# Performance work log

Hardware: AMD Instinct MI355X
Metric: run time of the kernel (lower is better)

## Reference

```python
import jax, jax.numpy as jnp
import numpy as np

N = 50000      # nodes
E = 640000     # edges
HID = 64       # hid_dim (per-head channels C)
HEADS = 4
D = HID * HEADS  # 256, conv output dim (concat=True)
LN_EPS = 1e-5


def setup_inputs() -> dict:
    key = jax.random.key(0)
    ks = jax.random.split(key, 10)
    def w(k, shape, scale=0.05):
        return jax.random.normal(k, shape, dtype=jnp.float32) * scale
    x = jax.random.normal(ks[0], (N, HID), dtype=jnp.float32)
    edge_index = jax.random.randint(ks[1], (2, E), 0, N)
    return {
        'x': x,
        'edge_index': edge_index,
        'Wq': w(ks[2], (D, HID)), 'bq': jnp.zeros((D,), jnp.float32),
        'Wk': w(ks[3], (D, HID)), 'bk': jnp.zeros((D,), jnp.float32),
        'Wv': w(ks[4], (D, HID)), 'bv': jnp.zeros((D,), jnp.float32),
        'Wskip': w(ks[5], (D, HID)), 'bskip': jnp.zeros((D,), jnp.float32),
        'Wbeta': w(ks[6], (1, 3 * D)),
        'ln_g': jnp.ones((D,), jnp.float32), 'ln_b': jnp.zeros((D,), jnp.float32),
        'Wproj': w(ks[7], (HID, D)), 'bproj': jnp.zeros((HID,), jnp.float32),
    }


def _layer(x, edge_index, Wq, bq, Wk, bk, Wv, bv, Wskip, bskip, Wbeta, ln_g, ln_b, Wproj, bproj):
    src, dst = edge_index[0], edge_index[1]  # message flows src -> dst
    # q/k/v projections, [N, H, C]
    q = (x @ Wq.T + bq).reshape(N, HEADS, HID)
    k = (x @ Wk.T + bk).reshape(N, HEADS, HID)
    v = (x @ Wv.T + bv).reshape(N, HEADS, HID)
    # edge-wise attention logits: [E, H]
    alpha = jnp.einsum('ehc,ehc->eh', q[dst], k[src]) / jnp.sqrt(jnp.float32(HID))
    # per-destination-node softmax (segment softmax)
    m = jax.ops.segment_max(alpha, dst, num_segments=N)          # [N, H]
    ex = jnp.exp(alpha - m[dst])                                 # [E, H]
    s = jax.ops.segment_sum(ex, dst, num_segments=N)             # [N, H]
    attn = ex / (s[dst] + 1e-16)                                 # [E, H]
    # weighted scatter-aggregate of values -> [N, H*C]
    msg = (v[src] * attn[..., None]).reshape(E, D)
    out = jax.ops.segment_sum(msg, dst, num_segments=N)          # [N, D]
    # beta gated skip (TransformerConv beta=True, root_weight=True)
    x_r = x @ Wskip.T + bskip                                    # [N, D]
    beta = jax.nn.sigmoid(jnp.concatenate([out, x_r, out - x_r], axis=-1) @ Wbeta.T)  # [N, 1]
    h = beta * x_r + (1.0 - beta) * out
    # LayerNorm over last dim
    mu = jnp.mean(h, axis=-1, keepdims=True)
    var = jnp.var(h, axis=-1, keepdims=True)
    h = (h - mu) * jax.lax.rsqrt(var + LN_EPS) * ln_g + ln_b
    # projection + residual + ReLU (dropout = identity in eval)
    h = h @ Wproj.T + bproj
    return jax.nn.relu(h + x)


def reference(x, edge_index, Wq, bq, Wk, bk, Wv, bv, Wskip, bskip, Wbeta, ln_g, ln_b, Wproj, bproj):
    return _layer(x, edge_index, Wq, bq, Wk, bk, Wv, bv, Wskip, bskip, Wbeta, ln_g, ln_b, Wproj, bproj)
```

## Files before the change

### kernel.cpp

```cpp
#include <hip/hip_runtime.h>
#include <stdint.h>

#define NND 50000
#define NED 640000

typedef unsigned short u16;
typedef unsigned int u32;
typedef __attribute__((ext_vector_type(8))) short short8;
typedef __attribute__((ext_vector_type(4))) float f32x4;
typedef __attribute__((ext_vector_type(2))) float fx2;

__device__ __forceinline__ float bf2f(u16 u) {
    union { u32 i; float f; } x; x.i = ((u32)u) << 16; return x.f;
}
__device__ __forceinline__ u16 f2bf(float f) {
    union { u32 i; float f; } x; x.f = f;
    u32 u = x.i;
    return (u16)((u + 0x7fffu + ((u >> 16) & 1u)) >> 16);
}
__device__ __forceinline__ float bflo(u32 w) {
    union { u32 i; float f; } x; x.i = w << 16; return x.f;
}
__device__ __forceinline__ float bfhi(u32 w) {
    union { u32 i; float f; } x; x.i = w & 0xffff0000u; return x.f;
}
__device__ __forceinline__ u32 pk2(float lo, float hi) {
    return (u32)f2bf(lo) | ((u32)f2bf(hi) << 16);
}
__device__ __forceinline__ u32 pk_fp8_4(u32 w0, u32 w1) {
    u32 p = __builtin_amdgcn_cvt_pk_fp8_f32(bflo(w0), bfhi(w0), 0, false);
    p = __builtin_amdgcn_cvt_pk_fp8_f32(bflo(w1), bfhi(w1), p, true);
    return p;
}
__device__ __forceinline__ void dec8v(u32 a, u32 b, fx2* f) {
    f[0] = __builtin_amdgcn_cvt_pk_f32_fp8(a, false);
    f[1] = __builtin_amdgcn_cvt_pk_f32_fp8(a, true);
    f[2] = __builtin_amdgcn_cvt_pk_f32_fp8(b, false);
    f[3] = __builtin_amdgcn_cvt_pk_f32_fp8(b, true);
}

__global__ void k_wt(const float* __restrict__ Wq, const float* __restrict__ Wk,
                     const float* __restrict__ Wv, const float* __restrict__ Ws,
                     const float* __restrict__ Wp,
                     const float* __restrict__ bq, const float* __restrict__ bk,
                     const float* __restrict__ bv, const float* __restrict__ bs,
                     u16* __restrict__ wb, float* __restrict__ bias_c,
                     u16* __restrict__ wpA, int* __restrict__ deg) {
    int idx = blockIdx.x * 256 + threadIdx.x;
    if (idx < 65536) {
        int j = idx & 7;
        int lane = (idx >> 3) & 63;
        int q = (idx >> 9) & 1;
        int dt = idx >> 10;
        int dim = dt * 16 + (lane & 15);
        int k = q * 32 + ((lane >> 4) & 3) * 8 + j;
        int mat = dim >> 8, r = dim & 255;
        const float* W = (mat == 0) ? Wq : (mat == 1) ? Wk : (mat == 2) ? Wv : Ws;
        float v = W[r * 64 + k] * ((mat == 0) ? 0.125f : 1.0f);
        wb[idx] = f2bf(v);
    } else if (idx < 65536 + 1024) {
        int dim = idx - 65536;
        int mat = dim >> 8, r = dim & 255;
        const float* B = (mat == 0) ? bq : (mat == 1) ? bk : (mat == 2) ? bv : bs;
        bias_c[dim] = B[r] * ((mat == 0) ? 0.125f : 1.0f);
    } else if (idx < 65536 + 1024 + 16384) {
        int w = idx - 66560;
        int j = w & 7;
        int lane = (w >> 3) & 63;
        int kc = (w >> 9) & 7;
        int mt = w >> 12;
        int dim = mt * 16 + (lane & 15);
        int k = kc * 32 + ((lane >> 4) & 3) * 8 + j;
        wpA[w] = f2bf(Wp[dim * 256 + k]);
    } else if (idx < 65536 + 1024 + 16384 + NND) {
        deg[idx - 82944] = 0;
    }
}

#define CNT_BLKS 2500
#define PPAD 1040
__global__ __launch_bounds__(256) void k_fillproj(
    const int* __restrict__ esrc, const int* __restrict__ edst,
    int* __restrict__ deg, int* __restrict__ csr,
    const float* __restrict__ x, const u16* __restrict__ wb,
    const float* __restrict__ bias_c,
    uint2* __restrict__ q8, uint4* __restrict__ kv8, u16* __restrict__ xr16)
{
    __shared__ u16 hb[16 * PPAD];
    if (blockIdx.x < CNT_BLKS) {
        int e = blockIdx.x * 256 + threadIdx.x;
        if (e < NED) {
            int d = edst[e];
            int pos = atomicAdd(&deg[d], 1);
            if (pos < 64) csr[(d << 6) + pos] = esrc[e];
        }
        return;
    }
    const int t = threadIdx.x;
    const int wave = t >> 6, lane = t & 63;
    const int node0 = (blockIdx.x - CNT_BLKS) * 16;
    const int lr = lane & 15, quad = lane >> 4;

    int node = node0 + lr;
    if (node > NND - 1) node = NND - 1;
    short8 xf0, xf1;
    {
        const float* xp = x + (size_t)node * 64 + quad * 8;
        float4 a = *reinterpret_cast<const float4*>(xp);
        float4 b = *reinterpret_cast<const float4*>(xp + 4);
        float4 c = *reinterpret_cast<const float4*>(xp + 32);
        float4 d = *reinterpret_cast<const float4*>(xp + 36);
        xf0[0] = (short)f2bf(a.x); xf0[1] = (short)f2bf(a.y);
        xf0[2] = (short)f2bf(a.z); xf0[3] = (short)f2bf(a.w);
        xf0[4] = (short)f2bf(b.x); xf0[5] = (short)f2bf(b.y);
        xf0[6] = (short)f2bf(b.z); xf0[7] = (short)f2bf(b.w);
        xf1[0] = (short)f2bf(c.x); xf1[1] = (short)f2bf(c.y);
        xf1[2] = (short)f2bf(c.z); xf1[3] = (short)f2bf(c.w);
        xf1[4] = (short)f2bf(d.x); xf1[5] = (short)f2bf(d.y);
        xf1[6] = (short)f2bf(d.z); xf1[7] = (short)f2bf(d.w);
    }
    #pragma unroll 4
    for (int dtl = 0; dtl < 16; ++dtl) {
        int dt = wave * 16 + dtl;
        const u16* wp = wb + (size_t)(dt * 2) * 512 + lane * 8;
        short8 a0 = *reinterpret_cast<const short8*>(wp);
        short8 a1 = *reinterpret_cast<const short8*>(wp + 512);
        f32x4 bias = *reinterpret_cast<const f32x4*>(bias_c + dt * 16 + quad * 4);
        f32x4 acc = {0.f, 0.f, 0.f, 0.f};
        acc = __builtin_amdgcn_mfma_f32_16x16x32_bf16(a0, xf0, acc, 0, 0, 0);
        acc = __builtin_amdgcn_mfma_f32_16x16x32_bf16(a1, xf1, acc, 0, 0, 0);
        uint2 st;
        st.x = pk2(acc[0] + bias[0], acc[1] + bias[1]);
        st.y = pk2(acc[2] + bias[2], acc[3] + bias[3]);
        *reinterpret_cast<uint2*>(&hb[lr * PPAD + dt * 16 + quad * 4]) = st;
    }
    __syncthreads();
    #pragma unroll
    for (int it = 0; it < 2; ++it) {
        int idx = it * 256 + t;
        int nip = idx >> 5, g = idx & 31;
        int gnode = node0 + nip;
        if (gnode < NND) {
            const u16* hp = &hb[nip * PPAD];
            *reinterpret_cast<uint4*>(xr16 + (size_t)gnode * 256 + g * 8) =
                *reinterpret_cast<const uint4*>(hp + 768 + g * 8);
            uint4 qw = *reinterpret_cast<const uint4*>(hp + g * 8);
            uint2 qs;
            qs.x = pk_fp8_4(qw.x, qw.y);
            qs.y = pk_fp8_4(qw.z, qw.w);
            q8[(size_t)gnode * 32 + g] = qs;
            uint4 kw = *reinterpret_cast<const uint4*>(hp + 256 + g * 8);
            uint4 vw = *reinterpret_cast<const uint4*>(hp + 512 + g * 8);
            uint4 kvs;
            kvs.x = pk_fp8_4(kw.x, kw.y);
            kvs.y = pk_fp8_4(kw.z, kw.w);
            kvs.z = pk_fp8_4(vw.x, vw.y);
            kvs.w = pk_fp8_4(vw.z, vw.w);
            kv8[(size_t)gnode * 32 + g] = kvs;
        }
    }
}

#define PS 264
#define NPB 16
__global__ __launch_bounds__(256) void k_attnepi(
    const int* __restrict__ deg, const int* __restrict__ csr,
    const uint2* __restrict__ q8, const uint4* __restrict__ kv8,
    const u16* __restrict__ xr16, const float* __restrict__ x,
    const float* __restrict__ Wbeta, const float* __restrict__ ln_g,
    const float* __restrict__ ln_b, const u16* __restrict__ wpA,
    const float* __restrict__ bproj, float* __restrict__ y)
{
    __shared__ u16 hn[NPB * PS];
    const int t = threadIdx.x;
    const int wave = __builtin_amdgcn_readfirstlane(t >> 6);
    const int lane = t & 63;
    const int sub = lane & 31, h = lane >> 5;
    const int es = (sub >> 4) & 1, dl = sub & 15;
    const int lr = lane & 15, grp = lane >> 4;
    const int base = blockIdx.x * NPB;

    int dg_[2], ia_[2], ib_[2];
    uint4 qv_[2];
    #pragma unroll
    for (int p = 0; p < 2; ++p) {
        int node = base + wave * 4 + 2 * p + h;
        int dgv = deg[node];
        dg_[p] = dgv > 64 ? 64 : dgv;
        ia_[p] = csr[(node << 6) + sub];
        ib_[p] = csr[(node << 6) + 32 + sub];
        qv_[p] = *reinterpret_cast<const uint4*>(
            reinterpret_cast<const char*>(q8) + (size_t)node * 256 + dl * 16);
    }
    const uint4* kvb = kv8 + (dl << 1);
    #pragma unroll
    for (int p = 0; p < 2; ++p) {
        const int dg = dg_[p];
        const int ia = ia_[p], ib = ib_[p];
        fx2 q[8];
        dec8v(qv_[p].x, qv_[p].y, q);
        dec8v(qv_[p].z, qv_[p].w, q + 4);
        int dgo = __shfl_xor(dg, 32);
        int mdg = __builtin_amdgcn_readfirstlane(dg > dgo ? dg : dgo);

        float s = 0.f;
        fx2 acc[8];
        #pragma unroll
        for (int r = 0; r < 8; ++r) acc[r] = fx2{0.f, 0.f};

        auto fetch = [&](int i, uint4& c0, uint4& c1) {
            int j = i + es;
            int lsrc = (h << 5) | (j & 31);
            int r0 = __shfl(ia, lsrc);
            int r1 = __shfl(ib, lsrc);
            int e = (j & 32) ? r1 : r0;
            if ((u32)e >= NND) e = 0;
            const uint4* kp = kvb + ((size_t)e << 5);
            c0 = kp[0];
            c1 = kp[1];
        };
        auto process = [&](int i, uint4 c0, uint4 c1) {
            int j = i + es;
            fx2 kk[8];
            dec8v(c0.x, c0.y, kk);
            dec8v(c1.x, c1.y, kk + 4);
            fx2 d0 = q[0] * kk[0] + q[1] * kk[1];
            fx2 d1 = q[2] * kk[2] + q[3] * kk[3];
            fx2 d2 = q[4] * kk[4] + q[5] * kk[5];
            fx2 d3 = q[6] * kk[6] + q[7] * kk[7];
            fx2 dd = (d0 + d1) + (d2 + d3);
            float pa = dd.x + dd.y;
            pa += __shfl_xor(pa, 1);
            pa += __shfl_xor(pa, 2);
            float ea = __expf(pa);
            ea = (j < dg) ? ea : 0.f;
            s += ea;
            fx2 ev = {ea, ea};
            fx2 vv[8];
            dec8v(c0.z, c0.w, vv);
            dec8v(c1.z, c1.w, vv + 4);
            acc[0] += ev * vv[0]; acc[1] += ev * vv[1];
            acc[2] += ev * vv[2]; acc[3] += ev * vv[3];
            acc[4] += ev * vv[4]; acc[5] += ev * vv[5];
            acc[6] += ev * vv[6]; acc[7] += ev * vv[7];
        };

        if (mdg > 0) {
            uint4 c0, c1, n0, n1;
            fetch(0, c0, c1);
            int i = 0;
            for (; i + 2 < mdg; i += 2) {
                fetch(i + 2, n0, n1);
                process(i, c0, c1);
                c0 = n0; c1 = n1;
            }
            process(i, c0, c1);
        }
        #pragma unroll
        for (int r = 0; r < 8; ++r) {
            acc[r].x += __shfl_xor(acc[r].x, 16);
            acc[r].y += __shfl_xor(acc[r].y, 16);
        }
        s += __shfl_xor(s, 16);
        float inv = 1.0f / (s + 1e-16f);
        if (es == 0) {
            int lid = wave * 4 + 2 * p + h;
            uint4 s0, s1;
            s0.x = pk2(acc[0].x * inv, acc[0].y * inv);
            s0.y = pk2(acc[1].x * inv, acc[1].y * inv);
            s0.z = pk2(acc[2].x * inv, acc[2].y * inv);
            s0.w = pk2(acc[3].x * inv, acc[3].y * inv);
            s1.x = pk2(acc[4].x * inv, acc[4].y * inv);
            s1.y = pk2(acc[5].x * inv, acc[5].y * inv);
            s1.z = pk2(acc[6].x * inv, acc[6].y * inv);
            s1.w = pk2(acc[7].x * inv, acc[7].y * inv);
            *reinterpret_cast<uint4*>(&hn[lid * PS + dl * 16]) = s0;
            *reinterpret_cast<uint4*>(&hn[lid * PS + dl * 16 + 8]) = s1;
        }
    }
    __syncthreads();

    {
        const float4* wb4 = reinterpret_cast<const float4*>(Wbeta);
        const float4* g44 = reinterpret_cast<const float4*>(ln_g);
        const float4* b44 = reinterpret_cast<const float4*>(ln_b);
        float wo[16], wx[16], wd[16], gg[16], bb[16];
        #pragma unroll
        for (int j = 0; j < 4; ++j) {
            float4 a = wb4[lr * 4 + j];
            float4 b = wb4[64 + lr * 4 + j];
            float4 c = wb4[128 + lr * 4 + j];
            float4 g = g44[lr * 4 + j];
            float4 bl = b44[lr * 4 + j];
            wo[j*4+0]=a.x; wo[j*4+1]=a.y; wo[j*4+2]=a.z; wo[j*4+3]=a.w;
            wx[j*4+0]=b.x; wx[j*4+1]=b.y; wx[j*4+2]=b.z; wx[j*4+3]=b.w;
            wd[j*4+0]=c.x; wd[j*4+1]=c.y; wd[j*4+2]=c.z; wd[j*4+3]=c.w;
            gg[j*4+0]=g.x; gg[j*4+1]=g.y; gg[j*4+2]=g.z; gg[j*4+3]=g.w;
            bb[j*4+0]=bl.x; bb[j*4+1]=bl.y; bb[j*4+2]=bl.z; bb[j*4+3]=bl.w;
        }
        int lid = wave * 4 + grp;
        int node = base + lid;
        {
            uint4 u0 = *reinterpret_cast<const uint4*>(&hn[lid * PS + lr * 16]);
            uint4 u1 = *reinterpret_cast<const uint4*>(&hn[lid * PS + lr * 16 + 8]);
            const uint4* xp = reinterpret_cast<const uint4*>(xr16 + (size_t)node * 256 + lr * 16);
            uint4 v0 = xp[0], v1 = xp[1];
            float o[16], r[16];
            o[0]=bflo(u0.x); o[1]=bfhi(u0.x); o[2]=bflo(u0.y); o[3]=bfhi(u0.y);
            o[4]=bflo(u0.z); o[5]=bfhi(u0.z); o[6]=bflo(u0.w); o[7]=bfhi(u0.w);
            o[8]=bflo(u1.x); o[9]=bfhi(u1.x); o[10]=bflo(u1.y); o[11]=bfhi(u1.y);
            o[12]=bflo(u1.z); o[13]=bfhi(u1.z); o[14]=bflo(u1.w); o[15]=bfhi(u1.w);
            r[0]=bflo(v0.x); r[1]=bfhi(v0.x); r[2]=bflo(v0.y); r[3]=bfhi(v0.y);
            r[4]=bflo(v0.z); r[5]=bfhi(v0.z); r[6]=bflo(v0.w); r[7]=bfhi(v0.w);
            r[8]=bflo(v1.x); r[9]=bfhi(v1.x); r[10]=bflo(v1.y); r[11]=bfhi(v1.y);
            r[12]=bflo(v1.z); r[13]=bfhi(v1.z); r[14]=bflo(v1.w); r[15]=bfhi(v1.w);
            float part = 0.f;
            #pragma unroll
            for (int cc = 0; cc < 16; ++cc)
                part = fmaf(wo[cc], o[cc], fmaf(wx[cc], r[cc], fmaf(wd[cc], o[cc]-r[cc], part)));
            part += __shfl_xor(part, 1); part += __shfl_xor(part, 2);
            part += __shfl_xor(part, 4); part += __shfl_xor(part, 8);
            float beta = 1.0f / (1.0f + __expf(-part));
            float hh[16];
            float sh = 0.f, sq = 0.f;
            #pragma unroll
            for (int cc = 0; cc < 16; ++cc) {
                hh[cc] = beta * r[cc] + (1.f - beta) * o[cc];
                sh += hh[cc];
                sq = fmaf(hh[cc], hh[cc], sq);
            }
            sh += __shfl_xor(sh, 1); sh += __shfl_xor(sh, 2);
            sh += __shfl_xor(sh, 4); sh += __shfl_xor(sh, 8);
            sq += __shfl_xor(sq, 1); sq += __shfl_xor(sq, 2);
            sq += __shfl_xor(sq, 4); sq += __shfl_xor(sq, 8);
            float mu = sh * (1.0f / 256.0f);
            float var = sq * (1.0f / 256.0f) - mu * mu;
            float ri = rsqrtf(var + 1e-5f);
            u32 pw[8];
            #pragma unroll
            for (int pp = 0; pp < 8; ++pp) {
                float z0 = (hh[pp*2+0] - mu) * ri * gg[pp*2+0] + bb[pp*2+0];
                float z1 = (hh[pp*2+1] - mu) * ri * gg[pp*2+1] + bb[pp*2+1];
                pw[pp] = pk2(z0, z1);
            }
            uint4 s0, s1;
            s0.x = pw[0]; s0.y = pw[1]; s0.z = pw[2]; s0.w = pw[3];
            s1.x = pw[4]; s1.y = pw[5]; s1.z = pw[6]; s1.w = pw[7];
            *reinterpret_cast<uint4*>(&hn[lid * PS + lr * 16]) = s0;
            *reinterpret_cast<uint4*>(&hn[lid * PS + lr * 16 + 8]) = s1;
        }
    }
    __syncthreads();

    {
        const int mt = wave;
        f32x4 acc = {0.f, 0.f, 0.f, 0.f};
        #pragma unroll
        for (int kc = 0; kc < 8; ++kc) {
            short8 a = *reinterpret_cast<const short8*>(wpA + ((size_t)(mt * 8 + kc) * 64 + lane) * 8);
            short8 b = *reinterpret_cast<const short8*>(&hn[lr * PS + kc * 32 + grp * 8]);
            acc = __builtin_amdgcn_mfma_f32_16x16x32_bf16(a, b, acc, 0, 0, 0);
        }
        int node = base + lr;
        {
            int d0 = mt * 16 + grp * 4;
            float4 bp4 = *reinterpret_cast<const float4*>(bproj + d0);
            float4 xv = *reinterpret_cast<const float4*>(x + (size_t)node * 64 + d0);
            float4 rr;
            rr.x = fmaxf(acc[0] + bp4.x + xv.x, 0.f);
            rr.y = fmaxf(acc[1] + bp4.y + xv.y, 0.f);
            rr.z = fmaxf(acc[2] + bp4.z + xv.z, 0.f);
            rr.w = fmaxf(acc[3] + bp4.w + xv.w, 0.f);
            *reinterpret_cast<float4*>(y + (size_t)node * 64 + d0) = rr;
        }
    }
}

extern "C" void kernel_launch(void* const* d_in, const int* in_sizes, int n_in,
                              void* d_out, int out_size, void* d_ws, size_t ws_size,
                              hipStream_t stream) {
    const float* x     = (const float*)d_in[0];
    const int*   eidx  = (const int*)d_in[1];
    const float* Wq    = (const float*)d_in[2];
    const float* bq    = (const float*)d_in[3];
    const float* Wk    = (const float*)d_in[4];
    const float* bk    = (const float*)d_in[5];
    const float* Wv    = (const float*)d_in[6];
    const float* bv    = (const float*)d_in[7];
    const float* Wsk   = (const float*)d_in[8];
    const float* bsk   = (const float*)d_in[9];
    const float* Wbeta = (const float*)d_in[10];
    const float* lng   = (const float*)d_in[11];
    const float* lnb   = (const float*)d_in[12];
    const float* Wp    = (const float*)d_in[13];
    const float* bp    = (const float*)d_in[14];
    float* y = (float*)d_out;

    char* ws = (char*)d_ws;
    size_t off = 0;
    auto alloc = [&](size_t b) { size_t o = off; off += (b + 255) & ~(size_t)255; return o; };
    uint2* q8   = (uint2*)(ws + alloc((size_t)NND * 256));
    uint4* kv8  = (uint4*)(ws + alloc((size_t)NND * 512));
    u16*  xr16  = (u16*)(ws + alloc((size_t)NND * 512));
    int* deg    = (int*)(ws + alloc((size_t)NND * 4));
    int* csr    = (int*)(ws + alloc((size_t)NND * 64 * 4));
    u16* wb     = (u16*)(ws + alloc((size_t)65536 * 2));
    float* bias_c = (float*)(ws + alloc((size_t)1024 * 4));
    u16* wpA    = (u16*)(ws + alloc((size_t)16384 * 2));

    k_wt      <<<520, 256, 0, stream>>>(Wq, Wk, Wv, Wsk, Wp, bq, bk, bv, bsk,
                                        wb, bias_c, wpA, deg);
    k_fillproj<<<CNT_BLKS + (NND + 15) / 16, 256, 0, stream>>>(
                 eidx, eidx + NED, deg, csr, x, wb, bias_c, q8, kv8, xr16);
    k_attnepi <<<(NND + NPB - 1) / NPB, 256, 0, stream>>>(deg, csr, q8, kv8, xr16, x,
                                                          Wbeta, lng, lnb, wpA, bp, y);
}
```

Before: 225.9 us.

## Shrink CSR to 16-bit indices, split K/V buffers, halve projection LDS

Stores the CSR neighbour indices as 16-bit values (node ids below 65536), so each node's adjacency list is fetched with one int load per lane and less memory traffic. The interleaved K/V fp8 buffer is split into separate K and V arrays, and the gather now issues one 16-byte load from each instead of two from the combined row. The projection kernel does its work in two passes through a half-size LDS tile (Q/K first, then V/skip), adding a barrier but lowering shared-memory use so more blocks can be resident. Bounds clamps are removed, so tail nodes rely on N being a multiple of 16, and the 16-bit ids only work while N stays below 65536.

```diff
diff --git a/kernel.cpp b/kernel.cpp
--- a/kernel.cpp
+++ b/kernel.cpp
@@ -10,9 +10,6 @@
 typedef __attribute__((ext_vector_type(4))) float f32x4;
 typedef __attribute__((ext_vector_type(2))) float fx2;
 
-__device__ __forceinline__ float bf2f(u16 u) {
-    union { u32 i; float f; } x; x.i = ((u32)u) << 16; return x.f;
-}
 __device__ __forceinline__ u16 f2bf(float f) {
     union { u32 i; float f; } x; x.f = f;
     u32 u = x.i;
@@ -78,21 +75,22 @@
 }
 
 #define CNT_BLKS 2500
-#define PPAD 1040
+#define PH 520
 __global__ __launch_bounds__(256) void k_fillproj(
     const int* __restrict__ esrc, const int* __restrict__ edst,
-    int* __restrict__ deg, int* __restrict__ csr,
+    int* __restrict__ deg, u16* __restrict__ csr,
     const float* __restrict__ x, const u16* __restrict__ wb,
     const float* __restrict__ bias_c,
-    uint2* __restrict__ q8, uint4* __restrict__ kv8, u16* __restrict__ xr16)
+    uint2* __restrict__ q8, uint2* __restrict__ k8, uint2* __restrict__ v8,
+    u16* __restrict__ xr16)
 {
-    __shared__ u16 hb[16 * PPAD];
+    __shared__ u16 hb[16 * PH];
     if (blockIdx.x < CNT_BLKS) {
         int e = blockIdx.x * 256 + threadIdx.x;
         if (e < NED) {
             int d = edst[e];
             int pos = atomicAdd(&deg[d], 1);
-            if (pos < 64) csr[(d << 6) + pos] = esrc[e];
+            if (pos < 64) csr[(d << 6) + pos] = (u16)esrc[e];
         }
         return;
     }
@@ -102,7 +100,6 @@
     const int lr = lane & 15, quad = lane >> 4;
 
     int node = node0 + lr;
-    if (node > NND - 1) node = NND - 1;
     short8 xf0, xf1;
     {
         const float* xp = x + (size_t)node * 64 + quad * 8;
@@ -119,9 +116,10 @@
         xf1[4] = (short)f2bf(d.x); xf1[5] = (short)f2bf(d.y);
         xf1[6] = (short)f2bf(d.z); xf1[7] = (short)f2bf(d.w);
     }
+
     #pragma unroll 4
-    for (int dtl = 0; dtl < 16; ++dtl) {
-        int dt = wave * 16 + dtl;
+    for (int dtl = 0; dtl < 8; ++dtl) {
+        int dt = wave * 8 + dtl;
         const u16* wp = wb + (size_t)(dt * 2) * 512 + lane * 8;
         short8 a0 = *reinterpret_cast<const short8*>(wp);
         short8 a1 = *reinterpret_cast<const short8*>(wp + 512);
@@ -132,7 +130,7 @@
         uint2 st;
         st.x = pk2(acc[0] + bias[0], acc[1] + bias[1]);
         st.y = pk2(acc[2] + bias[2], acc[3] + bias[3]);
-        *reinterpret_cast<uint2*>(&hb[lr * PPAD + dt * 16 + quad * 4]) = st;
+        *reinterpret_cast<uint2*>(&hb[lr * PH + dt * 16 + quad * 4]) = st;
     }
     __syncthreads();
     #pragma unroll
@@ -140,32 +138,58 @@
         int idx = it * 256 + t;
         int nip = idx >> 5, g = idx & 31;
         int gnode = node0 + nip;
-        if (gnode < NND) {
-            const u16* hp = &hb[nip * PPAD];
-            *reinterpret_cast<uint4*>(xr16 + (size_t)gnode * 256 + g * 8) =
-                *reinterpret_cast<const uint4*>(hp + 768 + g * 8);
-            uint4 qw = *reinterpret_cast<const uint4*>(hp + g * 8);
-            uint2 qs;
-            qs.x = pk_fp8_4(qw.x, qw.y);
-            qs.y = pk_fp8_4(qw.z, qw.w);
-            q8[(size_t)gnode * 32 + g] = qs;
-            uint4 kw = *reinterpret_cast<const uint4*>(hp + 256 + g * 8);
-            uint4 vw = *reinterpret_cast<const uint4*>(hp + 512 + g * 8);
-            uint4 kvs;
-            kvs.x = pk_fp8_4(kw.x, kw.y);
-            kvs.y = pk_fp8_4(kw.z, kw.w);
-            kvs.z = pk_fp8_4(vw.x, vw.y);
-            kvs.w = pk_fp8_4(vw.z, vw.w);
-            kv8[(size_t)gnode * 32 + g] = kvs;
-        }
+        const u16* hp = &hb[nip * PH];
+        uint4 qw = *reinterpret_cast<const uint4*>(hp + g * 8);
+        uint2 qs;
+        qs.x = pk_fp8_4(qw.x, qw.y);
+        qs.y = pk_fp8_4(qw.z, qw.w);
+        q8[(size_t)gnode * 32 + g] = qs;
+        uint4 kw = *reinterpret_cast<const uint4*>(hp + 256 + g * 8);
+        uint2 ks;
+        ks.x = pk_fp8_4(kw.x, kw.y);
+        ks.y = pk_fp8_4(kw.z, kw.w);
+        k8[(size_t)gnode * 32 + g] = ks;
+    }
+    __syncthreads();
+
+    #pragma unroll 4
+    for (int dtl = 0; dtl < 8; ++dtl) {
+        int dtg = 32 + wave * 8 + dtl;
+        const u16* wp = wb + (size_t)(dtg * 2) * 512 + lane * 8;
+        short8 a0 = *reinterpret_cast<const short8*>(wp);
+        short8 a1 = *reinterpret_cast<const short8*>(wp + 512);
+        f32x4 bias = *reinterpret_cast<const f32x4*>(bias_c + dtg * 16 + quad * 4);
+        f32x4 acc = {0.f, 0.f, 0.f, 0.f};
+        acc = __builtin_amdgcn_mfma_f32_16x16x32_bf16(a0, xf0, acc, 0, 0, 0);
+        acc = __builtin_amdgcn_mfma_f32_16x16x32_bf16(a1, xf1, acc, 0, 0, 0);
+        uint2 st;
+        st.x = pk2(acc[0] + bias[0], acc[1] + bias[1]);
+        st.y = pk2(acc[2] + bias[2], acc[3] + bias[3]);
+        *reinterpret_cast<uint2*>(&hb[lr * PH + (dtg - 32) * 16 + quad * 4]) = st;
+    }
+    __syncthreads();
+    #pragma unroll
+    for (int it = 0; it < 2; ++it) {
+        int idx = it * 256 + t;
+        int nip = idx >> 5, g = idx & 31;
+        int gnode = node0 + nip;
+        const u16* hp = &hb[nip * PH];
+        uint4 vw = *reinterpret_cast<const uint4*>(hp + g * 8);
+        uint2 vs;
+        vs.x = pk_fp8_4(vw.x, vw.y);
+        vs.y = pk_fp8_4(vw.z, vw.w);
+        v8[(size_t)gnode * 32 + g] = vs;
+        *reinterpret_cast<uint4*>(xr16 + (size_t)gnode * 256 + g * 8) =
+            *reinterpret_cast<const uint4*>(hp + 256 + g * 8);
     }
 }
 
 #define PS 264
 #define NPB 16
 __global__ __launch_bounds__(256) void k_attnepi(
-    const int* __restrict__ deg, const int* __restrict__ csr,
-    const uint2* __restrict__ q8, const uint4* __restrict__ kv8,
+    const int* __restrict__ deg, const u16* __restrict__ csr,
+    const uint2* __restrict__ q8, const uint2* __restrict__ k8,
+    const uint2* __restrict__ v8,
     const u16* __restrict__ xr16, const float* __restrict__ x,
     const float* __restrict__ Wbeta, const float* __restrict__ ln_g,
     const float* __restrict__ ln_b, const u16* __restrict__ wpA,
@@ -180,23 +204,23 @@
     const int lr = lane & 15, grp = lane >> 4;
     const int base = blockIdx.x * NPB;
 
-    int dg_[2], ia_[2], ib_[2];
+    int dg_[2], iw_[2];
     uint4 qv_[2];
     #pragma unroll
     for (int p = 0; p < 2; ++p) {
         int node = base + wave * 4 + 2 * p + h;
         int dgv = deg[node];
         dg_[p] = dgv > 64 ? 64 : dgv;
-        ia_[p] = csr[(node << 6) + sub];
-        ib_[p] = csr[(node << 6) + 32 + sub];
+        iw_[p] = reinterpret_cast<const int*>(csr)[node * 32 + sub];
         qv_[p] = *reinterpret_cast<const uint4*>(
             reinterpret_cast<const char*>(q8) + (size_t)node * 256 + dl * 16);
     }
-    const uint4* kvb = kv8 + (dl << 1);
+    const uint4* ku = reinterpret_cast<const uint4*>(k8) + dl;
+    const uint4* vu = reinterpret_cast<const uint4*>(v8) + dl;
     #pragma unroll
     for (int p = 0; p < 2; ++p) {
         const int dg = dg_[p];
-        const int ia = ia_[p], ib = ib_[p];
+        const int iw = iw_[p];
         fx2 q[8];
         dec8v(qv_[p].x, qv_[p].y, q);
         dec8v(qv_[p].z, qv_[p].w, q + 4);
@@ -208,22 +232,19 @@
         #pragma unroll
         for (int r = 0; r < 8; ++r) acc[r] = fx2{0.f, 0.f};
 
-        auto fetch = [&](int i, uint4& c0, uint4& c1) {
+        auto fetch = [&](int i, uint4& ck, uint4& cv) {
             int j = i + es;
-            int lsrc = (h << 5) | (j & 31);
-            int r0 = __shfl(ia, lsrc);
-            int r1 = __shfl(ib, lsrc);
-            int e = (j & 32) ? r1 : r0;
-            if ((u32)e >= NND) e = 0;
-            const uint4* kp = kvb + ((size_t)e << 5);
-            c0 = kp[0];
-            c1 = kp[1];
+            u32 w = (u32)__shfl(iw, (h << 5) | (j >> 1));
+            int e = (j & 1) ? (int)(w >> 16) : (int)(w & 0xffffu);
+            if (e >= NND) e = 0;
+            ck = ku[(size_t)e * 16];
+            cv = vu[(size_t)e * 16];
         };
-        auto process = [&](int i, uint4 c0, uint4 c1) {
+        auto process = [&](int i, uint4 ck, uint4 cv) {
             int j = i + es;
             fx2 kk[8];
-            dec8v(c0.x, c0.y, kk);
-            dec8v(c1.x, c1.y, kk + 4);
+            dec8v(ck.x, ck.y, kk);
+            dec8v(ck.z, ck.w, kk + 4);
             fx2 d0 = q[0] * kk[0] + q[1] * kk[1];
             fx2 d1 = q[2] * kk[2] + q[3] * kk[3];
             fx2 d2 = q[4] * kk[4] + q[5] * kk[5];
@@ -237,8 +258,8 @@
             s += ea;
             fx2 ev = {ea, ea};
             fx2 vv[8];
-            dec8v(c0.z, c0.w, vv);
-            dec8v(c1.z, c1.w, vv + 4);
+            dec8v(cv.x, cv.y, vv);
+            dec8v(cv.z, cv.w, vv + 4);
             acc[0] += ev * vv[0]; acc[1] += ev * vv[1];
             acc[2] += ev * vv[2]; acc[3] += ev * vv[3];
             acc[4] += ev * vv[4]; acc[5] += ev * vv[5];
@@ -246,15 +267,15 @@
         };
 
         if (mdg > 0) {
-            uint4 c0, c1, n0, n1;
-            fetch(0, c0, c1);
+            uint4 ck, cv, nk, nv;
+            fetch(0, ck, cv);
             int i = 0;
             for (; i + 2 < mdg; i += 2) {
-                fetch(i + 2, n0, n1);
-                process(i, c0, c1);
-                c0 = n0; c1 = n1;
+                fetch(i + 2, nk, nv);
+                process(i, ck, cv);
+                ck = nk; cv = nv;
             }
-            process(i, c0, c1);
+            process(i, ck, cv);
         }
         #pragma unroll
         for (int r = 0; r < 8; ++r) {
@@ -400,10 +421,11 @@
     size_t off = 0;
     auto alloc = [&](size_t b) { size_t o = off; off += (b + 255) & ~(size_t)255; return o; };
     uint2* q8   = (uint2*)(ws + alloc((size_t)NND * 256));
-    uint4* kv8  = (uint4*)(ws + alloc((size_t)NND * 512));
+    uint2* k8   = (uint2*)(ws + alloc((size_t)NND * 256));
+    uint2* v8   = (uint2*)(ws + alloc((size_t)NND * 256));
     u16*  xr16  = (u16*)(ws + alloc((size_t)NND * 512));
     int* deg    = (int*)(ws + alloc((size_t)NND * 4));
-    int* csr    = (int*)(ws + alloc((size_t)NND * 64 * 4));
+    u16* csr    = (u16*)(ws + alloc((size_t)NND * 64 * 2));
     u16* wb     = (u16*)(ws + alloc((size_t)65536 * 2));
     float* bias_c = (float*)(ws + alloc((size_t)1024 * 4));
     u16* wpA    = (u16*)(ws + alloc((size_t)16384 * 2));
@@ -411,7 +433,7 @@
     k_wt      <<<520, 256, 0, stream>>>(Wq, Wk, Wv, Wsk, Wp, bq, bk, bv, bsk,
                                         wb, bias_c, wpA, deg);
     k_fillproj<<<CNT_BLKS + (NND + 15) / 16, 256, 0, stream>>>(
-                 eidx, eidx + NED, deg, csr, x, wb, bias_c, q8, kv8, xr16);
-    k_attnepi <<<(NND + NPB - 1) / NPB, 256, 0, stream>>>(deg, csr, q8, kv8, xr16, x,
+                 eidx, eidx + NED, deg, csr, x, wb, bias_c, q8, k8, v8, xr16);
+    k_attnepi <<<(NND + NPB - 1) / NPB, 256, 0, stream>>>(deg, csr, q8, k8, v8, xr16, x,
                                                           Wbeta, lng, lnb, wpA, bp, y);
 }
```

Result: faster. 214.8 us (-4.9%).
